# Kernel tuning notes

Measured on AMD Instinct MI355X. Metric: run time of the kernel, lower is better.

The kernel has to match this reference:

```python
import jax, jax.numpy as jnp
import numpy as np

DIM = 768
NUM_HEADS = 12
HEAD_DIM = DIM // NUM_HEADS
SCALE = HEAD_DIM ** -0.5
B, N = 8, 1024


def setup_inputs() -> dict:
    key = jax.random.key(0)
    k1, k2, k3, k4, k5 = jax.random.split(key, 5)
    x = jax.random.normal(k1, (B, N, DIM), dtype=jnp.float32)
    # qkv: Linear(dim, 3*dim, bias=False); proj: Linear(dim, dim) with bias
    w_qkv = jax.random.normal(k2, (3 * DIM, DIM), dtype=jnp.float32) * (DIM ** -0.5)
    w_proj = jax.random.normal(k3, (DIM, DIM), dtype=jnp.float32) * (DIM ** -0.5)
    b_proj = jnp.zeros((DIM,), dtype=jnp.float32)
    # learned attention mask parameter, shape (H, L, L) with L >= N
    att_mask = jax.random.normal(k4, (NUM_HEADS, N, N), dtype=jnp.float32)
    return {"x": x, "w_qkv": w_qkv, "w_proj": w_proj, "b_proj": b_proj, "att_mask": att_mask}


def reference(x, w_qkv, w_proj, b_proj, att_mask):
    Bx, Nx, C = x.shape
    # qkv projection -> (3, B, H, N, head_dim)
    qkv = (x @ w_qkv.T).reshape(Bx, Nx, 3, NUM_HEADS, C // NUM_HEADS)
    qkv = jnp.transpose(qkv, (2, 0, 3, 1, 4))
    q, k, v = qkv[0], qkv[1], qkv[2]  # gpd_ratio==active_ratio==1 -> scaling factor 1
    # scores [B, H, N, N]
    attn = jnp.einsum('bhnd,bhmd->bhnm', q, k) * SCALE
    # custom sigmoid mask gating before softmax (broadcast over batch)
    attn = attn * jax.nn.sigmoid(att_mask[:, :Nx, :Nx])[None, :, :, :]
    attn = jax.nn.softmax(attn, axis=-1)
    out = jnp.einsum('bhnm,bhmd->bhnd', attn, v)
    out = jnp.transpose(out, (0, 2, 1, 3)).reshape(Bx, Nx, C)
    return out @ w_proj.T + b_proj
```

## Files before the change

kernel.cpp:

```cpp
#include <hip/hip_runtime.h>
#include <math.h>
#include <stdint.h>

typedef unsigned short u16;
typedef __attribute__((ext_vector_type(8))) short short8;
typedef __attribute__((ext_vector_type(4))) float f32x4;

#define GATE_SCALE 0.18033688011112042f

#if __has_builtin(__builtin_amdgcn_exp2f)
#define FEXP2(x) __builtin_amdgcn_exp2f(x)
#else
#define FEXP2(x) exp2f(x)
#endif

__device__ __forceinline__ u16 f2b(float f) {
    union { float f; unsigned u; } v; v.f = f;
    unsigned r = v.u + 0x7fffu + ((v.u >> 16) & 1u);
    return (u16)(r >> 16);
}
__device__ __forceinline__ u16 f2b_hu(float f) {
    union { float f; unsigned u; } v; v.f = f;
    return (u16)((v.u + 0x8000u) >> 16);
}
__device__ __forceinline__ float b2f(u16 u) {
    union { float f; unsigned u; } v; v.u = ((unsigned)u) << 16; return v.f;
}

#define GLL16(gsrc, ldsbase) __builtin_amdgcn_global_load_lds(                    \
    (__attribute__((address_space(1))) void*)(uintptr_t)(gsrc),                   \
    (__attribute__((address_space(3))) void*)(uint32_t)(uintptr_t)(ldsbase),      \
    16, 0, 0)

#define NX4  1572864
#define NW14 442368
#define NW24 147456
#define NXW4 (NX4 + NW14 + NW24)

__global__ __launch_bounds__(256) void prep_xw(
    const float4* __restrict__ x, const float4* __restrict__ wq,
    const float4* __restrict__ wp,
    ushort4* __restrict__ xb, ushort4* __restrict__ wqb,
    ushort4* __restrict__ wpb)
{
    size_t i = (size_t)blockIdx.x * 256 + threadIdx.x;
    float4 v; ushort4* dst; size_t j;
    if (i < NX4)            { j = i;               v = x[j];  dst = xb;  }
    else if (i < NX4 + NW14){ j = i - NX4;         v = wq[j]; dst = wqb; }
    else                    { j = i - (NX4 + NW14);v = wp[j]; dst = wpb; }
    ushort4 o; o.x = f2b(v.x); o.y = f2b(v.y); o.z = f2b(v.z); o.w = f2b(v.w);
    dst[j] = o;
}

__global__ __launch_bounds__(256) void prep_gate(
    const float* __restrict__ mask, u16* __restrict__ gp)
{
    const int bid = blockIdx.x;
    const int h = bid >> 8, qt = (bid >> 4) & 15, kt = bid & 15;
    const int t = threadIdx.x, l = t & 63, w = t >> 6;
    const int fq = l >> 4, fr = l & 15;
    const float* mb = mask + ((size_t)h * 1024 + qt * 64 + 16 * w + 4 * fq) * 1024
                           + kt * 64 + fr;
    union { u16 u[16]; float4 f[2]; } vals;
    #pragma unroll
    for (int i = 0; i < 4; ++i)
        #pragma unroll
        for (int nt = 0; nt < 4; ++nt) {
            float m = mb[(size_t)i * 1024 + nt * 16];
            vals.u[i * 4 + nt] = f2b(GATE_SCALE / (1.f + __expf(-m)));
        }
    float4* dst = (float4*)(gp + (size_t)bid * 4096 + (w * 64 + l) * 16);
    dst[0] = vals.f[0];
    dst[1] = vals.f[1];
}

__global__ __launch_bounds__(256) void qkv_gemm(
    const u16* __restrict__ xb, const u16* __restrict__ wb,
    u16* __restrict__ qb, u16* __restrict__ kb, u16* __restrict__ vb)
{
    __shared__ u16 As[128 * 32];
    __shared__ u16 Bs[128 * 32];
    const int t = threadIdx.x, l = t & 63, w = t >> 6;
    const int wm = (w & 1) * 64, wn = (w >> 1) * 64;
    const int m0 = blockIdx.y * 128, c0 = blockIdx.x * 128;

    f32x4 acc[4][4];
    #pragma unroll
    for (int i = 0; i < 4; ++i)
        #pragma unroll
        for (int j = 0; j < 4; ++j) { f32x4 z = {0.f,0.f,0.f,0.f}; acc[i][j] = z; }

    const int srow = l >> 2, sseg = l & 3;
    const int gcol = ((sseg ^ (srow & 3)) << 3);
    const u16* a0 = xb + (size_t)(m0 + w * 16 + srow) * 768 + gcol;
    const u16* a1 = a0 + (size_t)64 * 768;
    const u16* b0p = wb + (size_t)(c0 + w * 16 + srow) * 768 + gcol;
    const u16* b1p = b0p + (size_t)64 * 768;
    u16* ldsA0 = As + (w * 16) * 32;
    u16* ldsA1 = As + (64 + w * 16) * 32;
    u16* ldsB0 = Bs + (w * 16) * 32;
    u16* ldsB1 = Bs + (64 + w * 16) * 32;

    const int fr = l & 15, fq = l >> 4;
    const int fseg = (fq ^ (fr & 3)) << 3;

    for (int k0 = 0; k0 < 768; k0 += 32) {
        __syncthreads();
        GLL16(a0 + k0, ldsA0);
        GLL16(a1 + k0, ldsA1);
        GLL16(b0p + k0, ldsB0);
        GLL16(b1p + k0, ldsB1);
        __syncthreads();

        short8 af[4], bf[4];
        #pragma unroll
        for (int mt = 0; mt < 4; ++mt)
            af[mt] = *(const short8*)&As[(wm + mt * 16 + fr) * 32 + fseg];
        #pragma unroll
        for (int nt = 0; nt < 4; ++nt)
            bf[nt] = *(const short8*)&Bs[(wn + nt * 16 + fr) * 32 + fseg];
        #pragma unroll
        for (int mt = 0; mt < 4; ++mt)
            #pragma unroll
            for (int nt = 0; nt < 4; ++nt)
                acc[mt][nt] = __builtin_amdgcn_mfma_f32_16x16x32_bf16(
                    af[mt], bf[nt], acc[mt][nt], 0, 0, 0);
    }

    const int b = m0 >> 10;
    const int n0 = m0 & 1023;
    #pragma unroll
    for (int nt = 0; nt < 4; ++nt) {
        const int c = c0 + wn + nt * 16 + fr;
        const int which = c / 768;
        const int rem = c - which * 768;
        const int h = rem >> 6, d = rem & 63;
        if (which < 2) {
            u16* dst = ((which == 0) ? qb : kb)
                       + ((size_t)(b * 12 + h) * 1024) * 64 + d;
            #pragma unroll
            for (int mt = 0; mt < 4; ++mt)
                #pragma unroll
                for (int r = 0; r < 4; ++r) {
                    const int n = n0 + wm + mt * 16 + fq * 4 + r;
                    dst[(size_t)n * 64] = f2b(acc[mt][nt][r]);
                }
        } else {
            u16* dst = vb + ((size_t)(b * 12 + h) * 64 + d) * 1024
                          + n0 + wm + fq * 4;
            #pragma unroll
            for (int mt = 0; mt < 4; ++mt) {
                ushort4 pk;
                pk.x = f2b(acc[mt][nt][0]); pk.y = f2b(acc[mt][nt][1]);
                pk.z = f2b(acc[mt][nt][2]); pk.w = f2b(acc[mt][nt][3]);
                *(ushort4*)(dst + mt * 16) = pk;
            }
        }
    }
}

__global__ __launch_bounds__(256) void flash_attn(
    const u16* __restrict__ qb, const u16* __restrict__ kb,
    const u16* __restrict__ vt, const u16* __restrict__ gperm,
    u16* __restrict__ aob)
{
    __shared__ u16 Qs[4096], Ks[4096], Vts[4096], Ps[4096];
    const int t = threadIdx.x, l = t & 63, w = t >> 6;
    const int bid = blockIdx.x;
    const int h = bid >> 7, qt = (bid >> 3) & 15, b = bid & 7;
    const int q0 = qt * 64;
    const u16* hq = qb + (size_t)(b * 12 + h) * 65536;
    const u16* hk = kb + (size_t)(b * 12 + h) * 65536;
    const u16* hv = vt + (size_t)(b * 12 + h) * 65536;
    const u16* hg = gperm + (size_t)(h * 256 + qt * 16) * 4096 + (w * 64 + l) * 16;

    const int sr = l >> 3, ss = l & 7;
    const int sg = ((ss ^ (sr & 7)) << 3);
    const int j0 = w * 2, j1 = w * 2 + 1;

    GLL16(hq + (size_t)(q0 + j0 * 8 + sr) * 64 + sg, Qs + j0 * 512);
    GLL16(hq + (size_t)(q0 + j1 * 8 + sr) * 64 + sg, Qs + j1 * 512);

    float l_part[4] = {0.f, 0.f, 0.f, 0.f};
    f32x4 o[4];
    #pragma unroll
    for (int nt = 0; nt < 4; ++nt) { f32x4 z = {0.f,0.f,0.f,0.f}; o[nt] = z; }

    const int fq = l >> 4, fr = l & 15;
    const int sega = ((fq ^ (fr & 7)) << 3);
    const int segb = (((4 + fq) ^ (fr & 7)) << 3);

    for (int kt = 0; kt < 16; ++kt) {
        __syncthreads();
        GLL16(hk + (size_t)(kt * 64 + j0 * 8 + sr) * 64 + sg, Ks + j0 * 512);
        GLL16(hk + (size_t)(kt * 64 + j1 * 8 + sr) * 64 + sg, Ks + j1 * 512);
        GLL16(hv + (size_t)(j0 * 8 + sr) * 1024 + kt * 64 + sg, Vts + j0 * 512);
        GLL16(hv + (size_t)(j1 * 8 + sr) * 1024 + kt * 64 + sg, Vts + j1 * 512);
        const short8 g0 = *(const short8*)(hg + (size_t)kt * 4096);
        const short8 g1 = *(const short8*)(hg + (size_t)kt * 4096 + 8);
        __syncthreads();

        short8 aq0 = *(const short8*)&Qs[(16 * w + fr) * 64 + sega];
        short8 aq1 = *(const short8*)&Qs[(16 * w + fr) * 64 + segb];
        f32x4 sv[4];
        #pragma unroll
        for (int nt = 0; nt < 4; ++nt) {
            short8 k0f = *(const short8*)&Ks[(nt * 16 + fr) * 64 + sega];
            short8 k1f = *(const short8*)&Ks[(nt * 16 + fr) * 64 + segb];
            f32x4 z = {0.f,0.f,0.f,0.f};
            z = __builtin_amdgcn_mfma_f32_16x16x32_bf16(aq0, k0f, z, 0, 0, 0);
            z = __builtin_amdgcn_mfma_f32_16x16x32_bf16(aq1, k1f, z, 0, 0, 0);
            sv[nt] = z;
        }

        #pragma unroll
        for (int i = 0; i < 4; ++i) {
            const int pr = 4 * fq + i;
            #pragma unroll
            for (int nt = 0; nt < 4; ++nt) {
                const int idx = i * 4 + nt;
                const float g = b2f((u16)(idx < 8 ? g0[idx] : g1[idx - 8]));
                const float p = FEXP2(sv[nt][i] * g);
                l_part[i] += p;
                const int col = nt * 16 + fr;
                Ps[w * 1024 + pr * 64 + (((col >> 3) ^ (pr & 7)) << 3) + (col & 7)]
                    = f2b_hu(p);
            }
        }

        short8 ap0 = *(const short8*)&Ps[w * 1024 + fr * 64 + sega];
        short8 ap1 = *(const short8*)&Ps[w * 1024 + fr * 64 + segb];
        #pragma unroll
        for (int nt = 0; nt < 4; ++nt) {
            short8 v0 = *(const short8*)&Vts[(nt * 16 + fr) * 64 + sega];
            short8 v1 = *(const short8*)&Vts[(nt * 16 + fr) * 64 + segb];
            o[nt] = __builtin_amdgcn_mfma_f32_16x16x32_bf16(ap0, v0, o[nt], 0, 0, 0);
            o[nt] = __builtin_amdgcn_mfma_f32_16x16x32_bf16(ap1, v1, o[nt], 0, 0, 0);
        }
    }

    float l_i[4];
    #pragma unroll
    for (int i = 0; i < 4; ++i) {
        float s = l_part[i];
        s += __shfl_xor(s, 1, 16);
        s += __shfl_xor(s, 2, 16);
        s += __shfl_xor(s, 4, 16);
        s += __shfl_xor(s, 8, 16);
        l_i[i] = s;
    }

    #pragma unroll
    for (int i = 0; i < 4; ++i) {
        const float inv = 1.f / l_i[i];
        const int n = q0 + 16 * w + 4 * fq + i;
        const size_t rowoff = ((size_t)b * 1024 + n) * 768 + h * 64;
        #pragma unroll
        for (int nt = 0; nt < 4; ++nt)
            aob[rowoff + nt * 16 + fr] = f2b(o[nt][i] * inv);
    }
}

__global__ __launch_bounds__(256) void proj_gemm(
    const u16* __restrict__ aob, const u16* __restrict__ wb,
    const float* __restrict__ bproj, float* __restrict__ out)
{
    __shared__ u16 As[128 * 32];
    __shared__ u16 Bs[128 * 32];
    const int t = threadIdx.x, l = t & 63, w = t >> 6;
    const int wm = (w & 1) * 64, wn = (w >> 1) * 64;
    const int m0 = blockIdx.y * 128, c0 = blockIdx.x * 128;

    f32x4 acc[4][4];
    #pragma unroll
    for (int i = 0; i < 4; ++i)
        #pragma unroll
        for (int j = 0; j < 4; ++j) { f32x4 z = {0.f,0.f,0.f,0.f}; acc[i][j] = z; }

    const int srow = l >> 2, sseg = l & 3;
    const int gcol = ((sseg ^ (srow & 3)) << 3);
    const u16* a0 = aob + (size_t)(m0 + w * 16 + srow) * 768 + gcol;
    const u16* a1 = a0 + (size_t)64 * 768;
    const u16* b0p = wb + (size_t)(c0 + w * 16 + srow) * 768 + gcol;
    const u16* b1p = b0p + (size_t)64 * 768;
    u16* ldsA0 = As + (w * 16) * 32;
    u16* ldsA1 = As + (64 + w * 16) * 32;
    u16* ldsB0 = Bs + (w * 16) * 32;
    u16* ldsB1 = Bs + (64 + w * 16) * 32;

    const int fr = l & 15, fq = l >> 4;
    const int fseg = (fq ^ (fr & 3)) << 3;

    for (int k0 = 0; k0 < 768; k0 += 32) {
        __syncthreads();
        GLL16(a0 + k0, ldsA0);
        GLL16(a1 + k0, ldsA1);
        GLL16(b0p + k0, ldsB0);
        GLL16(b1p + k0, ldsB1);
        __syncthreads();

        short8 af[4], bf[4];
        #pragma unroll
        for (int mt = 0; mt < 4; ++mt)
            af[mt] = *(const short8*)&As[(wm + mt * 16 + fr) * 32 + fseg];
        #pragma unroll
        for (int nt = 0; nt < 4; ++nt)
            bf[nt] = *(const short8*)&Bs[(wn + nt * 16 + fr) * 32 + fseg];
        #pragma unroll
        for (int mt = 0; mt < 4; ++mt)
            #pragma unroll
            for (int nt = 0; nt < 4; ++nt)
                acc[mt][nt] = __builtin_amdgcn_mfma_f32_16x16x32_bf16(
                    af[mt], bf[nt], acc[mt][nt], 0, 0, 0);
    }

    #pragma unroll
    for (int nt = 0; nt < 4; ++nt) {
        const int c = c0 + wn + nt * 16 + fr;
        const float bias = bproj[c];
        #pragma unroll
        for (int mt = 0; mt < 4; ++mt)
            #pragma unroll
            for (int r = 0; r < 4; ++r) {
                const int m = m0 + wm + mt * 16 + fq * 4 + r;
                out[(size_t)m * 768 + c] = acc[mt][nt][r] + bias;
            }
    }
}

extern "C" void kernel_launch(void* const* d_in, const int* in_sizes, int n_in,
                              void* d_out, int out_size, void* d_ws, size_t ws_size,
                              hipStream_t stream)
{
    const float* x     = (const float*)d_in[0];
    const float* wqkv  = (const float*)d_in[1];
    const float* wproj = (const float*)d_in[2];
    const float* bproj = (const float*)d_in[3];
    const float* mask  = (const float*)d_in[4];
    float* out = (float*)d_out;

    char* ws = (char*)d_ws;
    u16* gperm  = (u16*)(ws);
    u16* xb     = (u16*)(ws + 25165824);
    u16* wqkvb  = (u16*)(ws + 37748736);
    u16* wprojb = (u16*)(ws + 41287680);
    u16* qb     = (u16*)(ws + 42467328);
    u16* kb     = (u16*)(ws + 55050240);
    u16* vb     = (u16*)(ws + 67633152);
    u16* aob    = (u16*)(ws + 80216064);

    prep_xw<<<NXW4 / 256, 256, 0, stream>>>(
        (const float4*)x, (const float4*)wqkv, (const float4*)wproj,
        (ushort4*)xb, (ushort4*)wqkvb, (ushort4*)wprojb);

    prep_gate<<<3072, 256, 0, stream>>>(mask, gperm);

    qkv_gemm<<<dim3(18, 64), 256, 0, stream>>>(xb, wqkvb, qb, kb, vb);

    flash_attn<<<1536, 256, 0, stream>>>(qb, kb, vb, gperm, aob);

    proj_gemm<<<dim3(6, 64), 256, 0, stream>>>(aob, wprojb, bproj, out);
}
```

Before: 248.2 us.

## Double-buffer LDS tiles in GEMM and attention kernels with a single barrier

Both GEMM kernels and the flash attention kernel now keep two shared-memory buffers per operand. Each iteration prefetches the next K/V (or A/B) tile, plus the next gate values, into the other buffer, then computes on the current one. This removes the second barrier per iteration and lets global-to-LDS loads overlap MFMA work. In exchange it doubles LDS use, which may lower occupancy, particularly for the attention kernel.

```diff
diff --git a/kernel.cpp b/kernel.cpp
--- a/kernel.cpp
+++ b/kernel.cpp
@@ -78,8 +78,8 @@
     const u16* __restrict__ xb, const u16* __restrict__ wb,
     u16* __restrict__ qb, u16* __restrict__ kb, u16* __restrict__ vb)
 {
-    __shared__ u16 As[128 * 32];
-    __shared__ u16 Bs[128 * 32];
+    __shared__ u16 As[2][4096];
+    __shared__ u16 Bs[2][4096];
     const int t = threadIdx.x, l = t & 63, w = t >> 6;
     const int wm = (w & 1) * 64, wn = (w >> 1) * 64;
     const int m0 = blockIdx.y * 128, c0 = blockIdx.x * 128;
@@ -96,29 +96,35 @@
     const u16* a1 = a0 + (size_t)64 * 768;
     const u16* b0p = wb + (size_t)(c0 + w * 16 + srow) * 768 + gcol;
     const u16* b1p = b0p + (size_t)64 * 768;
-    u16* ldsA0 = As + (w * 16) * 32;
-    u16* ldsA1 = As + (64 + w * 16) * 32;
-    u16* ldsB0 = Bs + (w * 16) * 32;
-    u16* ldsB1 = Bs + (64 + w * 16) * 32;
+    const int wofs = w * 512;
 
     const int fr = l & 15, fq = l >> 4;
     const int fseg = (fq ^ (fr & 3)) << 3;
 
-    for (int k0 = 0; k0 < 768; k0 += 32) {
+    GLL16(a0, &As[0][wofs]);
+    GLL16(a1, &As[0][2048 + wofs]);
+    GLL16(b0p, &Bs[0][wofs]);
+    GLL16(b1p, &Bs[0][2048 + wofs]);
+
+    for (int kt = 0; kt < 24; ++kt) {
         __syncthreads();
-        GLL16(a0 + k0, ldsA0);
-        GLL16(a1 + k0, ldsA1);
-        GLL16(b0p + k0, ldsB0);
-        GLL16(b1p + k0, ldsB1);
-        __syncthreads();
-
+        if (kt < 23) {
+            const int kn = (kt + 1) * 32;
+            const int nb = (kt + 1) & 1;
+            GLL16(a0 + kn, &As[nb][wofs]);
+            GLL16(a1 + kn, &As[nb][2048 + wofs]);
+            GLL16(b0p + kn, &Bs[nb][wofs]);
+            GLL16(b1p + kn, &Bs[nb][2048 + wofs]);
+        }
+        const u16* A = As[kt & 1];
+        const u16* B = Bs[kt & 1];
         short8 af[4], bf[4];
         #pragma unroll
         for (int mt = 0; mt < 4; ++mt)
-            af[mt] = *(const short8*)&As[(wm + mt * 16 + fr) * 32 + fseg];
+            af[mt] = *(const short8*)&A[(wm + mt * 16 + fr) * 32 + fseg];
         #pragma unroll
         for (int nt = 0; nt < 4; ++nt)
-            bf[nt] = *(const short8*)&Bs[(wn + nt * 16 + fr) * 32 + fseg];
+            bf[nt] = *(const short8*)&B[(wn + nt * 16 + fr) * 32 + fseg];
         #pragma unroll
         for (int mt = 0; mt < 4; ++mt)
             #pragma unroll
@@ -164,7 +170,7 @@
     const u16* __restrict__ vt, const u16* __restrict__ gperm,
     u16* __restrict__ aob)
 {
-    __shared__ u16 Qs[4096], Ks[4096], Vts[4096], Ps[4096];
+    __shared__ u16 Qs[4096], Ks[2][4096], Vts[2][4096], Ps[4096];
     const int t = threadIdx.x, l = t & 63, w = t >> 6;
     const int bid = blockIdx.x;
     const int h = bid >> 7, qt = (bid >> 3) & 15, b = bid & 7;
@@ -180,6 +186,13 @@
 
     GLL16(hq + (size_t)(q0 + j0 * 8 + sr) * 64 + sg, Qs + j0 * 512);
     GLL16(hq + (size_t)(q0 + j1 * 8 + sr) * 64 + sg, Qs + j1 * 512);
+    GLL16(hk + (size_t)(j0 * 8 + sr) * 64 + sg, &Ks[0][j0 * 512]);
+    GLL16(hk + (size_t)(j1 * 8 + sr) * 64 + sg, &Ks[0][j1 * 512]);
+    GLL16(hv + (size_t)(j0 * 8 + sr) * 1024 + sg, &Vts[0][j0 * 512]);
+    GLL16(hv + (size_t)(j1 * 8 + sr) * 1024 + sg, &Vts[0][j1 * 512]);
+
+    short8 g0 = *(const short8*)(hg);
+    short8 g1 = *(const short8*)(hg + 8);
 
     float l_part[4] = {0.f, 0.f, 0.f, 0.f};
     f32x4 o[4];
@@ -192,21 +205,28 @@
 
     for (int kt = 0; kt < 16; ++kt) {
         __syncthreads();
-        GLL16(hk + (size_t)(kt * 64 + j0 * 8 + sr) * 64 + sg, Ks + j0 * 512);
-        GLL16(hk + (size_t)(kt * 64 + j1 * 8 + sr) * 64 + sg, Ks + j1 * 512);
-        GLL16(hv + (size_t)(j0 * 8 + sr) * 1024 + kt * 64 + sg, Vts + j0 * 512);
-        GLL16(hv + (size_t)(j1 * 8 + sr) * 1024 + kt * 64 + sg, Vts + j1 * 512);
-        const short8 g0 = *(const short8*)(hg + (size_t)kt * 4096);
-        const short8 g1 = *(const short8*)(hg + (size_t)kt * 4096 + 8);
-        __syncthreads();
+        if (kt < 15) {
+            const int nb = (kt + 1) & 1;
+            const size_t ko = (size_t)(kt + 1) * 64;
+            GLL16(hk + (ko + j0 * 8 + sr) * 64 + sg, &Ks[nb][j0 * 512]);
+            GLL16(hk + (ko + j1 * 8 + sr) * 64 + sg, &Ks[nb][j1 * 512]);
+            GLL16(hv + (size_t)(j0 * 8 + sr) * 1024 + ko + sg, &Vts[nb][j0 * 512]);
+            GLL16(hv + (size_t)(j1 * 8 + sr) * 1024 + ko + sg, &Vts[nb][j1 * 512]);
+        }
+        const int ktn = (kt < 15) ? kt + 1 : 15;
+        short8 gn0 = *(const short8*)(hg + (size_t)ktn * 4096);
+        short8 gn1 = *(const short8*)(hg + (size_t)ktn * 4096 + 8);
+
+        const u16* Kc = Ks[kt & 1];
+        const u16* Vc = Vts[kt & 1];
 
         short8 aq0 = *(const short8*)&Qs[(16 * w + fr) * 64 + sega];
         short8 aq1 = *(const short8*)&Qs[(16 * w + fr) * 64 + segb];
         f32x4 sv[4];
         #pragma unroll
         for (int nt = 0; nt < 4; ++nt) {
-            short8 k0f = *(const short8*)&Ks[(nt * 16 + fr) * 64 + sega];
-            short8 k1f = *(const short8*)&Ks[(nt * 16 + fr) * 64 + segb];
+            short8 k0f = *(const short8*)&Kc[(nt * 16 + fr) * 64 + sega];
+            short8 k1f = *(const short8*)&Kc[(nt * 16 + fr) * 64 + segb];
             f32x4 z = {0.f,0.f,0.f,0.f};
             z = __builtin_amdgcn_mfma_f32_16x16x32_bf16(aq0, k0f, z, 0, 0, 0);
             z = __builtin_amdgcn_mfma_f32_16x16x32_bf16(aq1, k1f, z, 0, 0, 0);
@@ -232,11 +252,14 @@
         short8 ap1 = *(const short8*)&Ps[w * 1024 + fr * 64 + segb];
         #pragma unroll
         for (int nt = 0; nt < 4; ++nt) {
-            short8 v0 = *(const short8*)&Vts[(nt * 16 + fr) * 64 + sega];
-            short8 v1 = *(const short8*)&Vts[(nt * 16 + fr) * 64 + segb];
+            short8 v0 = *(const short8*)&Vc[(nt * 16 + fr) * 64 + sega];
+            short8 v1 = *(const short8*)&Vc[(nt * 16 + fr) * 64 + segb];
             o[nt] = __builtin_amdgcn_mfma_f32_16x16x32_bf16(ap0, v0, o[nt], 0, 0, 0);
             o[nt] = __builtin_amdgcn_mfma_f32_16x16x32_bf16(ap1, v1, o[nt], 0, 0, 0);
         }
+
+        g0 = gn0;
+        g1 = gn1;
     }
 
     float l_i[4];
@@ -265,8 +288,8 @@
     const u16* __restrict__ aob, const u16* __restrict__ wb,
     const float* __restrict__ bproj, float* __restrict__ out)
 {
-    __shared__ u16 As[128 * 32];
-    __shared__ u16 Bs[128 * 32];
+    __shared__ u16 As[2][4096];
+    __shared__ u16 Bs[2][4096];
     const int t = threadIdx.x, l = t & 63, w = t >> 6;
     const int wm = (w & 1) * 64, wn = (w >> 1) * 64;
     const int m0 = blockIdx.y * 128, c0 = blockIdx.x * 128;
@@ -283,29 +306,35 @@
     const u16* a1 = a0 + (size_t)64 * 768;
     const u16* b0p = wb + (size_t)(c0 + w * 16 + srow) * 768 + gcol;
     const u16* b1p = b0p + (size_t)64 * 768;
-    u16* ldsA0 = As + (w * 16) * 32;
-    u16* ldsA1 = As + (64 + w * 16) * 32;
-    u16* ldsB0 = Bs + (w * 16) * 32;
-    u16* ldsB1 = Bs + (64 + w * 16) * 32;
+    const int wofs = w * 512;
 
     const int fr = l & 15, fq = l >> 4;
     const int fseg = (fq ^ (fr & 3)) << 3;
 
-    for (int k0 = 0; k0 < 768; k0 += 32) {
+    GLL16(a0, &As[0][wofs]);
+    GLL16(a1, &As[0][2048 + wofs]);
+    GLL16(b0p, &Bs[0][wofs]);
+    GLL16(b1p, &Bs[0][2048 + wofs]);
+
+    for (int kt = 0; kt < 24; ++kt) {
         __syncthreads();
-        GLL16(a0 + k0, ldsA0);
-        GLL16(a1 + k0, ldsA1);
-        GLL16(b0p + k0, ldsB0);
-        GLL16(b1p + k0, ldsB1);
-        __syncthreads();
-
+        if (kt < 23) {
+            const int kn = (kt + 1) * 32;
+            const int nb = (kt + 1) & 1;
+            GLL16(a0 + kn, &As[nb][wofs]);
+            GLL16(a1 + kn, &As[nb][2048 + wofs]);
+            GLL16(b0p + kn, &Bs[nb][wofs]);
+            GLL16(b1p + kn, &Bs[nb][2048 + wofs]);
+        }
+        const u16* A = As[kt & 1];
+        const u16* B = Bs[kt & 1];
         short8 af[4], bf[4];
         #pragma unroll
         for (int mt = 0; mt < 4; ++mt)
-            af[mt] = *(const short8*)&As[(wm + mt * 16 + fr) * 32 + fseg];
+            af[mt] = *(const short8*)&A[(wm + mt * 16 + fr) * 32 + fseg];
         #pragma unroll
         for (int nt = 0; nt < 4; ++nt)
-            bf[nt] = *(const short8*)&Bs[(wn + nt * 16 + fr) * 32 + fseg];
+            bf[nt] = *(const short8*)&B[(wn + nt * 16 + fr) * 32 + fseg];
         #pragma unroll
         for (int mt = 0; mt < 4; ++mt)
             #pragma unroll
```

New measurement: 249.1 us. About the same (+0.4%).
